# Kernel tuning notes

Measured on AMD Instinct MI355X. Metric: run time of the kernel, lower is better.

The kernel has to match this reference:

```python
import jax, jax.numpy as jnp
import numpy as np

B, N, D = 2, 2048, 256
H = 8
HD = D // H
SCALE = HD ** 0.5  # NOTE: source MULTIPLIES by sqrt(head_dim)
EPS = 1e-5
DFF = 4 * D


def setup_inputs() -> dict:
    key = jax.random.key(0)
    ks = jax.random.split(key, 9)
    s = lambda fan_in: 1.0 / np.sqrt(fan_in)
    return {
        "x": jax.random.normal(ks[0], (B, N, D), dtype=jnp.float32),
        # weights stored [in, out] (transposed torch Linear)
        "qkv_w": jax.random.normal(ks[1], (D, 3 * D), dtype=jnp.float32) * s(D),
        "proj_w": jax.random.normal(ks[2], (D, D), dtype=jnp.float32) * s(D),
        "proj_b": jax.random.normal(ks[3], (D,), dtype=jnp.float32) * 0.01,
        "fc1_w": jax.random.normal(ks[4], (D, DFF), dtype=jnp.float32) * s(D),
        "fc1_b": jax.random.normal(ks[5], (DFF,), dtype=jnp.float32) * 0.01,
        "fc2_w": jax.random.normal(ks[6], (DFF, D), dtype=jnp.float32) * s(DFF),
        "fc2_b": jax.random.normal(ks[7], (D,), dtype=jnp.float32) * 0.01,
        "ln1_g": jnp.ones((D,), dtype=jnp.float32),
        "ln1_b": jnp.zeros((D,), dtype=jnp.float32),
    }


def _layernorm(x, g, b):
    mu = jnp.mean(x, axis=-1, keepdims=True)
    var = jnp.mean(jnp.square(x - mu), axis=-1, keepdims=True)
    return (x - mu) * jax.lax.rsqrt(var + EPS) * g + b


def reference(x, qkv_w, proj_w, proj_b, fc1_w, fc1_b, fc2_w, fc2_b, ln1_g, ln1_b):
    b, n, d = x.shape
    # --- MHA ---
    qkv = (x @ qkv_w).reshape(b, n, 3, H, HD)
    q = qkv[:, :, 0].transpose(0, 2, 1, 3)  # [B,H,N,HD]
    k = qkv[:, :, 1].transpose(0, 2, 1, 3)
    v = qkv[:, :, 2].transpose(0, 2, 1, 3)
    att = jnp.einsum("bhqd,bhkd->bhqk", q, k) * SCALE  # multiplied, per source
    att = jax.nn.softmax(att, axis=-1)
    out = jnp.einsum("bhqk,bhkd->bhqd", att, v)
    out = out.transpose(0, 2, 1, 3).reshape(b, n, d)
    out = out @ proj_w + proj_b
    # --- post-norm residual ---
    net = _layernorm(out + x, ln1_g, ln1_b)
    shortcut = net
    # --- MLP (NO activation in source forward) ---
    net = (net @ fc1_w + fc1_b) @ fc2_w + fc2_b
    return net + shortcut
```

## Files before the change

kernel.cpp:

```cpp
#include <hip/hip_runtime.h>


typedef __attribute__((ext_vector_type(8))) short short8;
typedef __attribute__((ext_vector_type(4))) short short4v;
typedef __attribute__((ext_vector_type(8))) _Float16 half8;
typedef __attribute__((ext_vector_type(4))) _Float16 half4;
typedef __attribute__((ext_vector_type(2))) __fp16 fp16x2;
typedef __attribute__((ext_vector_type(4))) float floatx4;
typedef __attribute__((ext_vector_type(2))) unsigned int uint2v;
typedef unsigned short u16;

#define MFMAG(a,b,c)  __builtin_amdgcn_mfma_f32_16x16x32_f16((a),(b),(c),0,0,0)
#if __has_builtin(__builtin_amdgcn_mfma_f32_16x16x16_f16)
#define MFMAPV(a,b,c) __builtin_amdgcn_mfma_f32_16x16x16_f16((a),(b),(c),0,0,0)
#else
#define MFMAPV(a,b,c) __builtin_amdgcn_mfma_f32_16x16x16f16((a),(b),(c),0,0,0)
#endif
#define CLF 8.1615404f

#if __has_builtin(__builtin_amdgcn_exp2f)
#define EX2(x) __builtin_amdgcn_exp2f(x)
#else
#define EX2(x) exp2f(x)
#endif

__device__ __forceinline__ float bf2f(u16 u) { return __uint_as_float(((unsigned)u) << 16); }
__device__ __forceinline__ float h2f(u16 u) { _Float16 h = *(_Float16*)&u; return (float)h; }
__device__ __forceinline__ u16 f2h(float f) { _Float16 h = (_Float16)f; return *(u16*)&h; }
__device__ __forceinline__ unsigned pkh2(float a, float b) {
#if __has_builtin(__builtin_amdgcn_cvt_pkrtz)
  fp16x2 h = __builtin_amdgcn_cvt_pkrtz(a, b);
  return *(unsigned*)&h;
#else
  return (unsigned)f2h(a) | ((unsigned)f2h(b) << 16);
#endif
}
__device__ __forceinline__ void gll16(const void* g, void* l) {
  __builtin_amdgcn_global_load_lds((const __attribute__((address_space(1))) void*)g,
                                   (__attribute__((address_space(3))) void*)l, 16, 0, 0);
}

__global__ __launch_bounds__(256) void qkvprep_k(
    const void* __restrict__ x, const void* __restrict__ qkv_w,
    const void* __restrict__ proj_w, const void* __restrict__ fc1_w,
    const void* __restrict__ fc2_w, const void* __restrict__ proj_b,
    const void* __restrict__ fc1_b, const void* __restrict__ fc2_b,
    const void* __restrict__ ln_g, const void* __restrict__ ln_b,
    u16* __restrict__ wt_proj, u16* __restrict__ wt_fc1, u16* __restrict__ wt_fc2,
    u16* __restrict__ b_proj, u16* __restrict__ b_fc1, u16* __restrict__ b_fc2,
    u16* __restrict__ g_ln, u16* __restrict__ bb_ln,
    u16* __restrict__ vt, u16* __restrict__ qf, u16* __restrict__ kf)
{
  __shared__ __align__(16) u16 lds[9728];
  const int tid = threadIdx.x;
  const int lane = tid & 63;
  const float probe = bf2f(((const u16*)qkv_w)[lane]);
  const bool f32 = __ballot(!(fabsf(probe) < 1000.0f)) != 0ull;
  const int bid = blockIdx.x;
  #define RD(p, i) (f32 ? ((const float*)(p))[i] : bf2f(((const u16*)(p))[i]))

  if (bid >= 768) {
    int idx = bid - 768;
    if (idx < 144) {
      u16 (*tr)[70] = (u16(*)[70])lds;
      const void* src; u16* dst; int Ns, Kt, tk, tn;
      if (idx < 16)      { src = proj_w; dst = wt_proj; Ns = 256;  Kt = 256;
                           tk = idx & 3;  tn = idx >> 2; }
      else if (idx < 80) { idx -= 16; src = fc1_w; dst = wt_fc1; Ns = 1024; Kt = 256;
                           tk = idx & 3;  tn = idx >> 2; }
      else               { idx -= 80; src = fc2_w; dst = wt_fc2; Ns = 256;  Kt = 1024;
                           tk = idx & 15; tn = idx >> 4; }
      const int k0 = tk * 64, n0v = tn * 64;
      const int r = tid >> 6, c = tid & 63;
#pragma unroll
      for (int p = 0; p < 16; ++p) {
        const int k = k0 + p * 4 + r;
        tr[c][p * 4 + r] = f2h(RD(src, (size_t)k * Ns + n0v + c));
      }
      __syncthreads();
#pragma unroll
      for (int p = 0; p < 16; ++p) {
        const int n = n0v + p * 4 + r;
        dst[(size_t)n * Kt + k0 + c] = tr[p * 4 + r][c];
      }
    } else {
      const int j = (idx - 144) * 256 + tid;
      if (j < 256)       b_proj[j]        = f2h(RD(proj_b, j));
      else if (j < 1280) b_fc1[j - 256]   = f2h(RD(fc1_b, j - 256));
      else if (j < 1536) b_fc2[j - 1280]  = f2h(RD(fc2_b, j - 1280));
      else if (j < 1792) g_ln[j - 1536]   = f2h(RD(ln_g, j - 1536));
      else if (j < 2048) bb_ln[j - 1792]  = f2h(RD(ln_b, j - 1792));
    }
    return;
  }
  #undef RD

  u16 (*As)[40] = (u16(*)[40])lds;
  u16 (*Bs)[40] = (u16(*)[40])(lds + 2560);
  u16* Vt = lds + 5120;
  const int mb = bid / 12, nb = bid % 12;
  const int m0 = mb * 64, n0 = nb * 64;
  const int wid = tid >> 6;
  const int wm = (wid >> 1) * 32, wn = (wid & 1) * 32;
  const int lm = lane & 15, quad = lane >> 4;

  floatx4 zero = {0.f, 0.f, 0.f, 0.f};
  floatx4 acc[2][2] = {{zero, zero}, {zero, zero}};

  const int arow = tid >> 2, aoff = (tid & 3) * 8;
  const int bn = tid & 63, bk8 = (tid >> 6) * 8;

  short8 rah, rbh;
  auto ld = [&](int kk) {
    if (f32) {
      const float* xp = (const float*)x + (size_t)(m0 + arow) * 256 + kk + aoff;
      floatx4 a0 = *(const floatx4*)xp;
      floatx4 a1 = *(const floatx4*)(xp + 4);
#pragma unroll
      for (int j = 0; j < 4; ++j) {
        rah[j]     = (short)f2h(a0[j]);
        rah[4 + j] = (short)f2h(a1[j]);
      }
      const float* wp = (const float*)qkv_w + (size_t)(kk + bk8) * 768 + n0 + bn;
#pragma unroll
      for (int j = 0; j < 8; ++j) rbh[j] = (short)f2h(wp[(size_t)j * 768]);
    } else {
      short8 a = *(const short8*)((const u16*)x + (size_t)(m0 + arow) * 256 + kk + aoff);
#pragma unroll
      for (int j = 0; j < 8; ++j) rah[j] = (short)f2h(bf2f((u16)a[j]));
      const u16* wp = (const u16*)qkv_w + (size_t)(kk + bk8) * 768 + n0 + bn;
#pragma unroll
      for (int j = 0; j < 8; ++j) rbh[j] = (short)f2h(bf2f(wp[(size_t)j * 768]));
    }
  };
  ld(0);
  for (int k0 = 0; k0 < 256; k0 += 32) {
    if (k0) __syncthreads();
    *(short8*)&As[arow][aoff] = rah;
    *(short8*)&Bs[bn][bk8] = rbh;
    __syncthreads();
    if (k0 + 32 < 256) ld(k0 + 32);
    half8 fa[2], fb[2];
#pragma unroll
    for (int t = 0; t < 2; ++t) {
      fa[t] = *(const half8*)&As[wm + t * 16 + lm][quad * 8];
      fb[t] = *(const half8*)&Bs[wn + t * 16 + lm][quad * 8];
    }
#pragma unroll
    for (int i = 0; i < 2; ++i)
#pragma unroll
      for (int j = 0; j < 2; ++j)
        acc[i][j] = MFMAG(fa[i], fb[j], acc[i][j]);
  }

  if (n0 >= 512) {
    __syncthreads();
#pragma unroll
    for (int i = 0; i < 2; ++i)
#pragma unroll
      for (int j = 0; j < 2; ++j)
#pragma unroll
        for (int r = 0; r < 4; ++r)
          Vt[(wn + j * 16 + lm) * 72 + wm + i * 16 + quad * 4 + r] = f2h(acc[i][j][r]);
    __syncthreads();
    const int bb = m0 >> 11, n = m0 & 2047;
#pragma unroll
    for (int pass = 0; pass < 2; ++pass) {
      const int dl = (tid >> 3) + pass * 32;
      const int oct = tid & 7;
      const int col = n0 - 512 + dl;
      const int d = col & 31, hh = col >> 5;
      short8 v = *(const short8*)&Vt[dl * 72 + oct * 8];
      *(short8*)&vt[(size_t)((bb * 8 + hh) * 32 + d) * 2048 + n + oct * 8] = v;
    }
    return;
  }

#pragma unroll
  for (int i = 0; i < 2; ++i) {
    const int rowb = m0 + wm + i * 16 + quad * 4;
#pragma unroll
    for (int j = 0; j < 2; ++j) {
      const int col = n0 + wn + j * 16 + lm;
#pragma unroll
      for (int r = 0; r < 4; ++r) {
        const int row = rowb + r;
        const u16 hv = f2h(acc[i][j][r]);
        if (col < 256) qf[(size_t)row * 256 + col] = hv;
        else           kf[(size_t)row * 256 + (col - 256)] = hv;
      }
    }
  }
}

__global__ __launch_bounds__(256) void prep_k(
    const void* __restrict__ x, const void* __restrict__ qkv_w,
    const void* __restrict__ proj_w, const void* __restrict__ fc1_w,
    const void* __restrict__ fc2_w, const void* __restrict__ proj_b,
    const void* __restrict__ fc1_b, const void* __restrict__ fc2_b,
    const void* __restrict__ ln_g, const void* __restrict__ ln_b,
    u16* __restrict__ x_f, u16* __restrict__ wq_f,
    u16* __restrict__ wt_proj, u16* __restrict__ wt_fc1, u16* __restrict__ wt_fc2,
    u16* __restrict__ b_proj, u16* __restrict__ b_fc1, u16* __restrict__ b_fc2,
    u16* __restrict__ g_ln, u16* __restrict__ bb_ln)
{
  __shared__ u16 tr[64][70];
  const int lane = threadIdx.x & 63;
  const float probe = bf2f(((const u16*)qkv_w)[lane]);
  const bool f32 = __ballot(!(fabsf(probe) < 1000.0f)) != 0ull;
  const int bid = blockIdx.x, tid = threadIdx.x;
  #define RD(p, i) (f32 ? ((const float*)(p))[i] : bf2f(((const u16*)(p))[i]))
  if (bid < 1024) {
    const size_t i = (size_t)bid * 1024 + tid * 4;
    const u16 o0 = f2h(RD(x, i)),     o1 = f2h(RD(x, i + 1));
    const u16 o2 = f2h(RD(x, i + 2)), o3 = f2h(RD(x, i + 3));
    short4v sv = {(short)o0, (short)o1, (short)o2, (short)o3};
    *(short4v*)&x_f[i] = sv;
  } else if (bid < 1216) {
    int idx = bid - 1024;
    const void* src; u16* dst; int Ns, Kt, tk, tn;
    if (idx < 48)       { src = qkv_w;  dst = wq_f;    Ns = 768;  Kt = 256;
                          tk = idx & 3;  tn = idx >> 2; }
    else if (idx < 64)  { idx -= 48;  src = proj_w; dst = wt_proj; Ns = 256; Kt = 256;
                          tk = idx & 3;  tn = idx >> 2; }
    else if (idx < 128) { idx -= 64;  src = fc1_w;  dst = wt_fc1;  Ns = 1024; Kt = 256;
                          tk = idx & 3;  tn = idx >> 2; }
    else                { idx -= 128; src = fc2_w;  dst = wt_fc2;  Ns = 256;  Kt = 1024;
                          tk = idx & 15; tn = idx >> 4; }
    const int k0 = tk * 64, n0 = tn * 64;
    const int r = tid >> 6, c = tid & 63;
#pragma unroll
    for (int p = 0; p < 16; ++p) {
      const int k = k0 + p * 4 + r;
      tr[c][p * 4 + r] = f2h(RD(src, (size_t)k * Ns + n0 + c));
    }
    __syncthreads();
#pragma unroll
    for (int p = 0; p < 16; ++p) {
      const int n = n0 + p * 4 + r;
      dst[(size_t)n * Kt + k0 + c] = tr[p * 4 + r][c];
    }
  } else {
    const int j = (bid - 1216) * 256 + tid;
    if (j < 256)       b_proj[j]        = f2h(RD(proj_b, j));
    else if (j < 1280) b_fc1[j - 256]   = f2h(RD(fc1_b, j - 256));
    else if (j < 1536) b_fc2[j - 1280]  = f2h(RD(fc2_b, j - 1280));
    else if (j < 1792) g_ln[j - 1536]   = f2h(RD(ln_g, j - 1536));
    else if (j < 2048) bb_ln[j - 1792]  = f2h(RD(ln_b, j - 1792));
  }
  #undef RD
}

template<int TW, int EPI, bool BIAS, bool RES, bool COMB>
__global__ __launch_bounds__(256) void gemm_k(
    const u16* __restrict__ A, const u16* __restrict__ Bt, const u16* __restrict__ A2,
    const u16* __restrict__ bias, const u16* __restrict__ res,
    void* __restrict__ out0, u16* __restrict__ aux1, u16* __restrict__ aux3,
    const float* __restrict__ muc,
    int M, int Nn, int K)
{
  constexpr int BT = TW * 32;
  constexpr int NC = TW / 2;
  __shared__ __align__(16) u16 As[BT][40];
  __shared__ __align__(16) u16 Bs[BT][40];
  __shared__ __align__(16) u16 Vt[(EPI == 2) ? 64 * 72 : 1];
  const int tid = threadIdx.x;
  const int m0 = blockIdx.y * BT, n0 = blockIdx.x * BT;
  const int wid = tid >> 6, lane = tid & 63;
  const int wm = (wid >> 1) * (TW * 16), wn = (wid & 1) * (TW * 16);
  const int lm = lane & 15, quad = lane >> 4;

  floatx4 zero = {0.f, 0.f, 0.f, 0.f};
  floatx4 acc[TW][TW];
#pragma unroll
  for (int i = 0; i < TW; ++i)
#pragma unroll
    for (int j = 0; j < TW; ++j) acc[i][j] = zero;

  auto comb8 = [&](int t, int col8) -> short8 {
    const size_t o = (size_t)t * 256 + col8;
    const int h = col8 >> 5;
    const float m0_ = muc[t * 8 + h],          m1_ = muc[32768 + t * 8 + h];
    const float m2_ = muc[65536 + t * 8 + h],  m3_ = muc[98304 + t * 8 + h];
    const float M = fmaxf(fmaxf(m0_, m1_), fmaxf(m2_, m3_));
    float w0 = EX2(m0_ - M), w1 = EX2(m1_ - M), w2 = EX2(m2_ - M), w3 = EX2(m3_ - M);
    const float inv = 1.f / (w0 + w1 + w2 + w3);
    w0 *= inv; w1 *= inv; w2 *= inv; w3 *= inv;
    short8 a0 = *(const short8*)&A[o],  a1 = *(const short8*)&A[o + 1048576];
    short8 a2 = *(const short8*)&A2[o], a3 = *(const short8*)&A2[o + 1048576];
    float v[8];
#pragma unroll
    for (int j = 0; j < 8; ++j)
      v[j] = w0 * h2f((u16)a0[j]) + w1 * h2f((u16)a1[j])
           + w2 * h2f((u16)a2[j]) + w3 * h2f((u16)a3[j]);
    uint2v uu0 = {pkh2(v[0], v[1]), pkh2(v[2], v[3])};
    uint2v uu1 = {pkh2(v[4], v[5]), pkh2(v[6], v[7])};
    short8 r;
    *(uint2v*)&r = uu0; *((uint2v*)&r + 1) = uu1;
    return r;
  };

  int srow[NC], soff[NC];
#pragma unroll
  for (int c = 0; c < NC; ++c) {
    const int cid = tid * NC + c;
    srow[c] = cid >> 2; soff[c] = (cid & 3) * 8;
  }

  short8 ra0[NC], rb0[NC];
  auto ld = [&](int kk) {
#pragma unroll
    for (int c = 0; c < NC; ++c) {
      rb0[c] = *(const short8*)&Bt[(size_t)(n0 + srow[c]) * K + kk + soff[c]];
      if (COMB) ra0[c] = comb8(m0 + srow[c], kk + soff[c]);
      else      ra0[c] = *(const short8*)&A[(size_t)(m0 + srow[c]) * K + kk + soff[c]];
    }
  };
  ld(0);
  for (int k0 = 0; k0 < K; k0 += 32) {
    if (k0) __syncthreads();
#pragma unroll
    for (int c = 0; c < NC; ++c) {
      *(short8*)&As[srow[c]][soff[c]] = ra0[c];
      *(short8*)&Bs[srow[c]][soff[c]] = rb0[c];
    }
    __syncthreads();
    if (k0 + 32 < K) ld(k0 + 32);
    half8 fa[TW], fb[TW];
#pragma unroll
    for (int t = 0; t < TW; ++t) {
      fa[t] = *(const half8*)&As[wm + t * 16 + lm][quad * 8];
      fb[t] = *(const half8*)&Bs[wn + t * 16 + lm][quad * 8];
    }
#pragma unroll
    for (int i = 0; i < TW; ++i)
#pragma unroll
      for (int j = 0; j < TW; ++j)
        acc[i][j] = MFMAG(fa[i], fb[j], acc[i][j]);
  }

  if (EPI == 2 && n0 >= 512) {
    __syncthreads();
#pragma unroll
    for (int i = 0; i < TW; ++i)
#pragma unroll
      for (int j = 0; j < TW; ++j)
#pragma unroll
        for (int r = 0; r < 4; ++r)
          Vt[(wn + j * 16 + lm) * 72 + wm + i * 16 + quad * 4 + r] = f2h(acc[i][j][r]);
    __syncthreads();
    const int bb = m0 >> 11, n = m0 & 2047;
#pragma unroll
    for (int pass = 0; pass < 2; ++pass) {
      const int dl = (tid >> 3) + pass * 32;
      const int oct = tid & 7;
      const int col = n0 - 512 + dl;
      const int d = col & 31, hh = col >> 5;
      short8 v = *(const short8*)&Vt[dl * 72 + oct * 8];
      *(short8*)&((u16*)out0)[(size_t)((bb * 8 + hh) * 32 + d) * 2048 + n + oct * 8] = v;
    }
    return;
  }

#pragma unroll
  for (int i = 0; i < TW; ++i) {
    const int rowb = m0 + wm + i * 16 + quad * 4;
#pragma unroll
    for (int j = 0; j < TW; ++j) {
      const int col = n0 + wn + j * 16 + lm;
      const float bv = BIAS ? h2f(bias[col]) : 0.f;
#pragma unroll
      for (int r = 0; r < 4; ++r) {
        const int row = rowb + r;
        float v = acc[i][j][r] + bv;
        const size_t o = (size_t)row * Nn + col;
        if (RES) v += h2f(res[o]);
        if (EPI == 0) {
          ((float*)out0)[o] = v;
        } else if (EPI == 1) {
          ((u16*)out0)[o] = f2h(v);
        } else {
          if (col < 256) aux1[(size_t)row * 256 + col] = f2h(v);
          else           aux3[(size_t)row * 256 + (col - 256)] = f2h(v);
        }
      }
    }
  }
}

__global__ __launch_bounds__(512) void gemm8_k(
    const u16* __restrict__ A, const u16* __restrict__ Bt,
    const u16* __restrict__ bias, const u16* __restrict__ res,
    float* __restrict__ out0, int Nn, int K)
{
  __shared__ __align__(16) u16 As[64][40];
  __shared__ __align__(16) u16 Bs[64][40];
  const int tid = threadIdx.x;
  const int m0 = blockIdx.y * 64, n0 = blockIdx.x * 64;
  const int wid = tid >> 6, lane = tid & 63;
  const int wm = (wid & 3) * 16, wn = (wid >> 2) * 32;
  const int lm = lane & 15, quad = lane >> 4;

  floatx4 zero = {0.f, 0.f, 0.f, 0.f};
  floatx4 acc0 = zero, acc1 = zero;

  const int sgrp = tid >> 8, stid = tid & 255;
  const int srow = stid >> 2, soff = (stid & 3) * 8;
  const u16* sp = sgrp ? Bt : A;
  const int sbase = sgrp ? n0 : m0;

  short8 rr;
  rr = *(const short8*)&sp[(size_t)(sbase + srow) * K + soff];
  for (int k0 = 0; k0 < K; k0 += 32) {
    if (k0) __syncthreads();
    if (sgrp) *(short8*)&Bs[srow][soff] = rr;
    else      *(short8*)&As[srow][soff] = rr;
    __syncthreads();
    if (k0 + 32 < K)
      rr = *(const short8*)&sp[(size_t)(sbase + srow) * K + k0 + 32 + soff];
    half8 fa = *(const half8*)&As[wm + lm][quad * 8];
    half8 fb0 = *(const half8*)&Bs[wn + lm][quad * 8];
    half8 fb1 = *(const half8*)&Bs[wn + 16 + lm][quad * 8];
    acc0 = MFMAG(fa, fb0, acc0);
    acc1 = MFMAG(fa, fb1, acc1);
  }

  const int rowb = m0 + wm + quad * 4;
  const int col0 = n0 + wn + lm, col1 = col0 + 16;
  const float bv0 = h2f(bias[col0]), bv1 = h2f(bias[col1]);
#pragma unroll
  for (int r = 0; r < 4; ++r) {
    const int row = rowb + r;
    const size_t o0 = (size_t)row * Nn + col0;
    const size_t o1 = (size_t)row * Nn + col1;
    out0[o0] = acc0[r] + bv0 + h2f(res[o0]);
    out0[o1] = acc1[r] + bv1 + h2f(res[o1]);
  }
}

__global__ __launch_bounds__(512) void projln8_k(
    const u16* __restrict__ A,
    const u16* __restrict__ A2,
    const u16* __restrict__ Bt,
    const u16* __restrict__ bias,
    const void* __restrict__ xraw,
    const void* __restrict__ probew,
    const u16* __restrict__ g, const u16* __restrict__ bb,
    const float* __restrict__ muc,
    u16* __restrict__ net)
{
  __shared__ __align__(16) u16 As[16][40];
  __shared__ __align__(16) u16 Bs[256][40];
  __shared__ float ss[8][16], ssq[8][16];
  const int tid = threadIdx.x;
  const int m0 = blockIdx.x * 16;
  const int wid = tid >> 6, lane = tid & 63;
  const int lm = lane & 15, quad = lane >> 4;
  const float probe = bf2f(((const u16*)probew)[lane]);
  const bool f32 = __ballot(!(fabsf(probe) < 1000.0f)) != 0ull;

  floatx4 zero = {0.f, 0.f, 0.f, 0.f};
  floatx4 acc0 = zero, acc1 = zero;

  auto comb8 = [&](int t, int col8) -> short8 {
    const size_t o = (size_t)t * 256 + col8;
    const int h = col8 >> 5;
    const float m0_ = muc[t * 8 + h],          m1_ = muc[32768 + t * 8 + h];
    const float m2_ = muc[65536 + t * 8 + h],  m3_ = muc[98304 + t * 8 + h];
    const float M = fmaxf(fmaxf(m0_, m1_), fmaxf(m2_, m3_));
    float w0 = EX2(m0_ - M), w1 = EX2(m1_ - M), w2 = EX2(m2_ - M), w3 = EX2(m3_ - M);
    const float inv = 1.f / (w0 + w1 + w2 + w3);
    w0 *= inv; w1 *= inv; w2 *= inv; w3 *= inv;
    short8 a0 = *(const short8*)&A[o],  a1 = *(const short8*)&A[o + 1048576];
    short8 a2 = *(const short8*)&A2[o], a3 = *(const short8*)&A2[o + 1048576];
    float v[8];
#pragma unroll
    for (int j = 0; j < 8; ++j)
      v[j] = w0 * h2f((u16)a0[j]) + w1 * h2f((u16)a1[j])
           + w2 * h2f((u16)a2[j]) + w3 * h2f((u16)a3[j]);
    uint2v uu0 = {pkh2(v[0], v[1]), pkh2(v[2], v[3])};
    uint2v uu1 = {pkh2(v[4], v[5]), pkh2(v[6], v[7])};
    short8 r;
    *(uint2v*)&r = uu0; *((uint2v*)&r + 1) = uu1;
    return r;
  };

  const int arow = lane >> 2, aoff = (lane & 3) * 8;
  int brow0 = wid * 32 + (lane >> 2), brow1 = brow0 + 16;
  const int boff = (lane & 3) * 8;

  short8 ra, rb0, rb1;
  if (wid == 0) ra = comb8(m0 + arow, aoff);
  rb0 = *(const short8*)&Bt[(size_t)brow0 * 256 + boff];
  rb1 = *(const short8*)&Bt[(size_t)brow1 * 256 + boff];

  for (int k0 = 0; k0 < 256; k0 += 32) {
    if (k0) __syncthreads();
    if (wid == 0) *(short8*)&As[arow][aoff] = ra;
    *(short8*)&Bs[brow0][boff] = rb0;
    *(short8*)&Bs[brow1][boff] = rb1;
    __syncthreads();
    if (k0 + 32 < 256) {
      if (wid == 0) ra = comb8(m0 + arow, k0 + 32 + aoff);
      rb0 = *(const short8*)&Bt[(size_t)brow0 * 256 + k0 + 32 + boff];
      rb1 = *(const short8*)&Bt[(size_t)brow1 * 256 + k0 + 32 + boff];
    }
    half8 fa = *(const half8*)&As[lm][quad * 8];
    half8 fb0 = *(const half8*)&Bs[wid * 32 + lm][quad * 8];
    half8 fb1 = *(const half8*)&Bs[wid * 32 + 16 + lm][quad * 8];
    acc0 = MFMAG(fa, fb0, acc0);
    acc1 = MFMAG(fa, fb1, acc1);
  }

  const int col0 = wid * 32 + lm, col1 = col0 + 16;
  const float bv0 = h2f(bias[col0]), bv1 = h2f(bias[col1]);
  float s[4], sq[4], v0[4], v1[4];
#pragma unroll
  for (int r = 0; r < 4; ++r) {
    const int row = quad * 4 + r;
    const size_t o0 = (size_t)(m0 + row) * 256 + col0;
    const size_t o1 = (size_t)(m0 + row) * 256 + col1;
    const float x0 = f32 ? ((const float*)xraw)[o0] : bf2f(((const u16*)xraw)[o0]);
    const float x1 = f32 ? ((const float*)xraw)[o1] : bf2f(((const u16*)xraw)[o1]);
    const float a = acc0[r] + bv0 + h2f(f2h(x0));
    const float b = acc1[r] + bv1 + h2f(f2h(x1));
    v0[r] = a; v1[r] = b;
    s[r] = a + b; sq[r] = a * a + b * b;
  }
#pragma unroll
  for (int d = 1; d < 16; d <<= 1)
#pragma unroll
    for (int r = 0; r < 4; ++r) {
      s[r] += __shfl_xor(s[r], d);
      sq[r] += __shfl_xor(sq[r], d);
    }
  if (lm == 0)
#pragma unroll
    for (int r = 0; r < 4; ++r) { ss[wid][quad * 4 + r] = s[r]; ssq[wid][quad * 4 + r] = sq[r]; }
  __syncthreads();
#pragma unroll
  for (int r = 0; r < 4; ++r) {
    const int row = quad * 4 + r;
    float ts = 0.f, tq = 0.f;
#pragma unroll
    for (int w = 0; w < 8; ++w) { ts += ss[w][row]; tq += ssq[w][row]; }
    const float mean = ts * (1.f / 256.f);
    const float var = tq * (1.f / 256.f) - mean * mean;
    const float is = rsqrtf(var + 1e-5f);
    net[(size_t)(m0 + row) * 256 + col0] =
        f2h((v0[r] - mean) * is * h2f(g[col0]) + h2f(bb[col0]));
    net[(size_t)(m0 + row) * 256 + col1] =
        f2h((v1[r] - mean) * is * h2f(g[col1]) + h2f(bb[col1]));
  }
}

template<int CHUNKS>
__global__ __launch_bounds__(256) void attn_k(
    const u16* __restrict__ qf16, const u16* __restrict__ kf16,
    const u16* __restrict__ vt, u16* __restrict__ outp, u16* __restrict__ out23,
    float* __restrict__ mu)
{
  __shared__ __align__(16) u16 Ks[2][64][32];
  __shared__ __align__(16) u16 Vs[2][32][64];
  const int tid = threadIdx.x, wid = tid >> 6, lane = tid & 63;
  const int lm = lane & 15, quad = lane >> 4;
  const int bid = blockIdx.x;
  const int chunk = (CHUNKS > 1) ? (bid >> 9) : 0;
  const int qblk = bid & 31, bh = (bid >> 5) & 15;
  const int b = bh >> 3, h = bh & 7;
  const int q0 = qblk * 64 + wid * 16;
  const size_t tb = (size_t)b * 2048;
  const int NT = 32 / CHUNKS;
  const int kofs = chunk * (2048 / CHUNKS);

  half8 qh;
  { size_t off = (tb + q0 + lm) * 256 + h * 32 + quad * 8;
    qh = *(const half8*)&qf16[off]; }

  const int kkey = tid >> 2, kg = tid & 3;
  const size_t kb = (tb + kofs + kkey) * 256 + h * 32 + kg * 8;
  const int vd = tid >> 3, vp = tid & 7, vk8 = vp ^ (vd & 7);
  const size_t vb = (size_t)(bh * 32 + vd) * 2048 + kofs + vk8 * 8;

  gll16(kf16 + kb, (u16*)Ks + tid * 8);
  gll16(vt  + vb,  (u16*)Vs + tid * 8);

  float mrun = -1e30f, lrun = 0.f;
  floatx4 o0 = {0.f,0.f,0.f,0.f}, o1 = {0.f,0.f,0.f,0.f};

  for (int kt = 0; kt < NT; ++kt) {
    const int buf = kt & 1;
    __syncthreads();
    if (kt < NT - 1) {
      const int nb = (buf ^ 1) * 2048;
      const size_t ko = (size_t)(kt + 1) * 16384;
      const size_t vo = (size_t)(kt + 1) * 64;
      gll16(kf16 + kb + ko, (u16*)Ks + nb + tid * 8);
      gll16(vt  + vb + vo,  (u16*)Vs + nb + tid * 8);
    }

    floatx4 z[4];
#pragma unroll
    for (int kf = 0; kf < 4; ++kf) {
      half8 khf = *(const half8*)&Ks[buf][kf * 16 + lm][quad * 8];
      floatx4 zz = {0.f,0.f,0.f,0.f};
      z[kf] = MFMAG(khf, qh, zz);
    }
    float zm = fmaxf(fmaxf(fmaxf(z[0][0], z[0][1]), fmaxf(z[0][2], z[0][3])),
               fmaxf(fmaxf(z[1][0], z[1][1]), fmaxf(z[1][2], z[1][3])));
    zm = fmaxf(zm, fmaxf(fmaxf(fmaxf(z[2][0], z[2][1]), fmaxf(z[2][2], z[2][3])),
                   fmaxf(fmaxf(z[3][0], z[3][1]), fmaxf(z[3][2], z[3][3]))));
    zm = fmaxf(zm, __shfl_xor(zm, 16));
    zm = fmaxf(zm, __shfl_xor(zm, 32));
    const float mn = fmaxf(mrun, zm);
    const float alpha = EX2((mrun - mn) * CLF);
    const float mc = mn * CLF;
    mrun = mn;
    float ls = 0.f;
    half4 pb[4];
#pragma unroll
    for (int kf = 0; kf < 4; ++kf) {
      const float p0 = EX2(__builtin_fmaf(z[kf][0], CLF, -mc));
      const float p1 = EX2(__builtin_fmaf(z[kf][1], CLF, -mc));
      const float p2 = EX2(__builtin_fmaf(z[kf][2], CLF, -mc));
      const float p3 = EX2(__builtin_fmaf(z[kf][3], CLF, -mc));
      ls += (p0 + p1) + (p2 + p3);
      uint2v uu = {pkh2(p0, p1), pkh2(p2, p3)};
      pb[kf] = *(half4*)&uu;
    }
    ls += __shfl_xor(ls, 16);
    ls += __shfl_xor(ls, 32);
    lrun = lrun * alpha + ls;
#pragma unroll
    for (int r = 0; r < 4; ++r) { o0[r] *= alpha; o1[r] *= alpha; }
    const u16* vbase = (const u16*)Vs + buf * 2048;
#pragma unroll
    for (int kf = 0; kf < 4; ++kf) {
      const int k8 = 2 * kf + (quad >> 1);
      const int d0 = lm, d1 = 16 + lm;
      half4 vf0 = *(const half4*)(vbase + (d0 * 8 + (k8 ^ (d0 & 7))) * 8 + (quad & 1) * 4);
      half4 vf1 = *(const half4*)(vbase + (d1 * 8 + (k8 ^ (d1 & 7))) * 8 + (quad & 1) * 4);
      o0 = MFMAPV(vf0, pb[kf], o0);
      o1 = MFMAPV(vf1, pb[kf], o1);
    }
  }
  const float inv = 1.0f / lrun;
  const size_t tok = tb + q0 + lm;
  u16* dst = ((CHUNKS > 2 && chunk >= 2) ? out23 : outp) + (size_t)(chunk & 1) * 1048576;
  const size_t rowo = tok * 256 + h * 32;
#pragma unroll
  for (int r = 0; r < 4; ++r) {
    dst[rowo + quad * 4 + r]      = f2h(o0[r] * inv);
    dst[rowo + 16 + quad * 4 + r] = f2h(o1[r] * inv);
  }
  if (CHUNKS > 1 && quad == 0)
    mu[chunk * 32768 + tok * 8 + h] = __builtin_fmaf(mrun, CLF, __log2f(lrun));
}

template<int CHUNKS>
__global__ __launch_bounds__(256) void combine_k(u16* __restrict__ d,
                                                 const u16* __restrict__ e,
                                                 const float* __restrict__ mu)
{
  const int t = blockIdx.x, c = threadIdx.x, h = c >> 5;
  const size_t o = (size_t)t * 256 + c;
  float m[CHUNKS];
  float M = -1e30f;
#pragma unroll
  for (int i = 0; i < CHUNKS; ++i) { m[i] = mu[i * 32768 + t * 8 + h]; M = fmaxf(M, m[i]); }
  float wsum = 0.f, acc = 0.f;
#pragma unroll
  for (int i = 0; i < CHUNKS; ++i) {
    const float w = EX2(m[i] - M);
    const u16 v = (i < 2) ? d[o + (size_t)i * 1048576] : e[o + (size_t)(i - 2) * 1048576];
    wsum += w; acc += w * h2f(v);
  }
  d[o] = f2h(acc / wsum);
}

__global__ __launch_bounds__(256) void ln_k(const float* __restrict__ pf,
                                            const u16* __restrict__ xh,
                                            const u16* __restrict__ g,
                                            const u16* __restrict__ bta,
                                            u16* __restrict__ net)
{
  const int t = blockIdx.x, c = threadIdx.x;
  const size_t o = (size_t)t * 256 + c;
  float v = pf[o] + h2f(xh[o]);
  float s = v, s2 = v * v;
#pragma unroll
  for (int d = 1; d < 64; d <<= 1) { s += __shfl_xor(s, d); s2 += __shfl_xor(s2, d); }
  __shared__ float ss[4], ss2[4];
  const int w = c >> 6;
  if ((c & 63) == 0) { ss[w] = s; ss2[w] = s2; }
  __syncthreads();
  s = ss[0] + ss[1] + ss[2] + ss[3];
  s2 = ss2[0] + ss2[1] + ss2[2] + ss2[3];
  const float mu = s * (1.f / 256.f);
  const float var = s2 * (1.f / 256.f) - mu * mu;
  const float is = rsqrtf(var + 1e-5f);
  net[o] = f2h((v - mu) * is * h2f(g[c]) + h2f(bta[c]));
}

extern "C" void kernel_launch(void* const* d_in, const int* in_sizes, int n_in,
                              void* d_out, int out_size, void* d_ws, size_t ws_size,
                              hipStream_t stream) {
  const void* x      = d_in[0];
  const void* qkv_w  = d_in[1];
  const void* proj_w = d_in[2];
  const void* proj_b = d_in[3];
  const void* fc1_w  = d_in[4];
  const void* fc1_b  = d_in[5];
  const void* fc2_w  = d_in[6];
  const void* fc2_b  = d_in[7];
  const void* ln_g   = d_in[8];
  const void* ln_b   = d_in[9];

  char* ws = (char*)d_ws;
  u16* b_proj  = (u16*)(ws + 4096);
  u16* b_fc1   = (u16*)(ws + 8192);
  u16* b_fc2   = (u16*)(ws + 12288);
  u16* g_ln    = (u16*)(ws + 16384);
  u16* bb_ln   = (u16*)(ws + 20480);
  u16* wq_f    = (u16*)(ws + 131072);
  u16* wt_proj = (u16*)(ws + 524288);
  u16* wt_fc1  = (u16*)(ws + 655360);
  u16* wt_fc2  = (u16*)(ws + 1179648);
  u16* x_f     = (u16*)(ws + 2097152);
  u16* q_f16   = (u16*)(ws + 4194304);
  u16* k_f16   = (u16*)(ws + 6291456);
  u16* vt      = (u16*)(ws + 8388608);
  float* mu    = (float*)(ws + 10485760);
  u16* out23   = (u16*)(ws + 11010048);
  u16* attn    = (u16*)d_out;

  u16* net4    = (u16*)(ws + 2097152);
  u16* hbuf4   = (u16*)(ws + 4194304);

  float* projf = (float*)(ws + 4194304);
  u16* net     = (u16*)(ws + 11010048);
  u16* hbuf    = (u16*)(ws + 2097152);

  const bool sk4 = ws_size >= 15204352;
  const bool sk2 = ws_size >= 11010048;

  if (sk4) {
    qkvprep_k<<<920, 256, 0, stream>>>(x, qkv_w, proj_w, fc1_w, fc2_w,
                                       proj_b, fc1_b, fc2_b, ln_g, ln_b,
                                       wt_proj, wt_fc1, wt_fc2,
                                       b_proj, b_fc1, b_fc2, g_ln, bb_ln,
                                       vt, q_f16, k_f16);
    attn_k<4><<<2048, 256, 0, stream>>>(q_f16, k_f16, vt, attn, out23, mu);
    projln8_k<<<256, 512, 0, stream>>>(attn, out23, wt_proj, b_proj, x, qkv_w,
                                       g_ln, bb_ln, mu, net4);
    gemm_k<2, 1, true, false, false><<<dim3(16, 64), 256, 0, stream>>>(
        net4, wt_fc1, nullptr, b_fc1, nullptr, hbuf4, nullptr, nullptr, nullptr,
        4096, 1024, 256);
    gemm8_k<<<dim3(4, 64), 512, 0, stream>>>(
        hbuf4, wt_fc2, b_fc2, net4, (float*)d_out, 256, 1024);
    return;
  }

  prep_k<<<1224, 256, 0, stream>>>(x, qkv_w, proj_w, fc1_w, fc2_w,
                                   proj_b, fc1_b, fc2_b, ln_g, ln_b,
                                   x_f, wq_f, wt_proj, wt_fc1, wt_fc2,
                                   b_proj, b_fc1, b_fc2, g_ln, bb_ln);
  gemm_k<2, 2, false, false, false><<<dim3(12, 64), 256, 0, stream>>>(
      x_f, wq_f, nullptr, nullptr, nullptr, vt, q_f16, k_f16, nullptr, 4096, 768, 256);
  if (sk2) {
    attn_k<2><<<1024, 256, 0, stream>>>(q_f16, k_f16, vt, attn, nullptr, mu);
    combine_k<2><<<4096, 256, 0, stream>>>(attn, nullptr, mu);
    gemm_k<2, 0, true, false, false><<<dim3(4, 64), 256, 0, stream>>>(
        attn, wt_proj, nullptr, b_proj, nullptr, projf, nullptr, nullptr, nullptr,
        4096, 256, 256);
  } else {
    attn_k<1><<<512, 256, 0, stream>>>(q_f16, k_f16, vt, attn, nullptr, nullptr);
    gemm_k<2, 0, true, false, false><<<dim3(4, 64), 256, 0, stream>>>(
        attn, wt_proj, nullptr, b_proj, nullptr, projf, nullptr, nullptr, nullptr,
        4096, 256, 256);
  }
  ln_k<<<4096, 256, 0, stream>>>(projf, x_f, g_ln, bb_ln, net);
  gemm_k<2, 1, true, false, false><<<dim3(16, 64), 256, 0, stream>>>(
      net, wt_fc1, nullptr, b_fc1, nullptr, hbuf, nullptr, nullptr, nullptr,
      4096, 1024, 256);
  gemm_k<2, 0, true, true, false><<<dim3(4, 64), 256, 0, stream>>>(
      hbuf, wt_fc2, nullptr, b_fc2, net, d_out, nullptr, nullptr, nullptr,
      4096, 256, 1024);
}
```

Baseline: 141.2 us.

## Fold linear MLP into single precomputed weight matrix and bias

The MLP has no activation, so fc1 and fc2 collapse into one 256x256 matrix (fc1_w·fc2_w) and a combined bias (fc1_b·fc2_w + fc2_b). Both are computed inside the prep kernel using extra MFMA blocks. The two large MLP GEMMs over 4096 rows become one 256-wide GEMM with residual. The fused weight is recomputed on every call and rounded to fp16, which changes the rounding behaviour.

```diff
diff --git a/kernel.cpp b/kernel.cpp
--- a/kernel.cpp
+++ b/kernel.cpp
@@ -46,9 +46,8 @@
     const void* __restrict__ fc2_w, const void* __restrict__ proj_b,
     const void* __restrict__ fc1_b, const void* __restrict__ fc2_b,
     const void* __restrict__ ln_g, const void* __restrict__ ln_b,
-    u16* __restrict__ wt_proj, u16* __restrict__ wt_fc1, u16* __restrict__ wt_fc2,
-    u16* __restrict__ b_proj, u16* __restrict__ b_fc1, u16* __restrict__ b_fc2,
-    u16* __restrict__ g_ln, u16* __restrict__ bb_ln,
+    u16* __restrict__ wt_proj, u16* __restrict__ wmlp, u16* __restrict__ bmlp,
+    u16* __restrict__ b_proj, u16* __restrict__ g_ln, u16* __restrict__ bb_ln,
     u16* __restrict__ vt, u16* __restrict__ qf, u16* __restrict__ kf)
 {
   __shared__ __align__(16) u16 lds[9728];
@@ -61,39 +60,91 @@
 
   if (bid >= 768) {
     int idx = bid - 768;
-    if (idx < 144) {
+    if (idx < 16) {
       u16 (*tr)[70] = (u16(*)[70])lds;
-      const void* src; u16* dst; int Ns, Kt, tk, tn;
-      if (idx < 16)      { src = proj_w; dst = wt_proj; Ns = 256;  Kt = 256;
-                           tk = idx & 3;  tn = idx >> 2; }
-      else if (idx < 80) { idx -= 16; src = fc1_w; dst = wt_fc1; Ns = 1024; Kt = 256;
-                           tk = idx & 3;  tn = idx >> 2; }
-      else               { idx -= 80; src = fc2_w; dst = wt_fc2; Ns = 256;  Kt = 1024;
-                           tk = idx & 15; tn = idx >> 4; }
+      const int tk = idx & 3, tn = idx >> 2;
       const int k0 = tk * 64, n0v = tn * 64;
       const int r = tid >> 6, c = tid & 63;
 #pragma unroll
       for (int p = 0; p < 16; ++p) {
         const int k = k0 + p * 4 + r;
-        tr[c][p * 4 + r] = f2h(RD(src, (size_t)k * Ns + n0v + c));
+        tr[c][p * 4 + r] = f2h(RD(proj_w, (size_t)k * 256 + n0v + c));
       }
       __syncthreads();
 #pragma unroll
       for (int p = 0; p < 16; ++p) {
         const int n = n0v + p * 4 + r;
-        dst[(size_t)n * Kt + k0 + c] = tr[p * 4 + r][c];
+        wt_proj[(size_t)n * 256 + k0 + c] = tr[p * 4 + r][c];
       }
+    } else if (idx < 32) {
+      idx -= 16;
+      const int tn = idx >> 2, tk2 = idx & 3;
+      const int n0v = tn * 64, k0v = tk2 * 64;
+      u16 (*As)[40] = (u16(*)[40])lds;
+      u16 (*Bs)[40] = (u16(*)[40])(lds + 2560);
+      const int wid = tid >> 6;
+      const int wm = (wid >> 1) * 32, wn = (wid & 1) * 32;
+      const int lm = lane & 15, quad = lane >> 4;
+      floatx4 zero = {0.f, 0.f, 0.f, 0.f};
+      floatx4 acc[2][2] = {{zero, zero}, {zero, zero}};
+      const int an = tid & 63, aj8 = (tid >> 6) * 8;
+      const int bk = tid >> 2, bj8 = (tid & 3) * 8;
+      short8 ra, rb;
+      auto ld = [&](int j0) {
+#pragma unroll
+        for (int jj = 0; jj < 8; ++jj)
+          ra[jj] = (short)f2h(RD(fc2_w, (size_t)(j0 + aj8 + jj) * 256 + n0v + an));
+#pragma unroll
+        for (int jj = 0; jj < 8; ++jj)
+          rb[jj] = (short)f2h(RD(fc1_w, (size_t)(k0v + bk) * 1024 + j0 + bj8 + jj));
+      };
+      ld(0);
+      for (int j0 = 0; j0 < 1024; j0 += 32) {
+        if (j0) __syncthreads();
+        *(short8*)&As[an][aj8] = ra;
+        *(short8*)&Bs[bk][bj8] = rb;
+        __syncthreads();
+        if (j0 + 32 < 1024) ld(j0 + 32);
+        half8 fa[2], fb[2];
+#pragma unroll
+        for (int t = 0; t < 2; ++t) {
+          fa[t] = *(const half8*)&As[wm + t * 16 + lm][quad * 8];
+          fb[t] = *(const half8*)&Bs[wn + t * 16 + lm][quad * 8];
+        }
+#pragma unroll
+        for (int i = 0; i < 2; ++i)
+#pragma unroll
+          for (int j = 0; j < 2; ++j)
+            acc[i][j] = MFMAG(fa[i], fb[j], acc[i][j]);
+      }
+#pragma unroll
+      for (int i = 0; i < 2; ++i) {
+        const int rown = n0v + wm + i * 16 + quad * 4;
+#pragma unroll
+        for (int j = 0; j < 2; ++j) {
+          const int colk = k0v + wn + j * 16 + lm;
+#pragma unroll
+          for (int r = 0; r < 4; ++r)
+            wmlp[(size_t)(rown + r) * 256 + colk] = f2h(acc[i][j][r]);
+        }
+      }
+    } else if (idx < 36) {
+      const int q = idx - 32;
+      const int n = q * 64 + (tid >> 2), jg = tid & 3;
+      float s = 0.f;
+#pragma unroll 8
+      for (int j = jg; j < 1024; j += 4)
+        s += RD(fc1_b, j) * RD(fc2_w, (size_t)j * 256 + n);
+      s += __shfl_xor(s, 1);
+      s += __shfl_xor(s, 2);
+      if (jg == 0) bmlp[n] = f2h(s + RD(fc2_b, n));
     } else {
-      const int j = (idx - 144) * 256 + tid;
-      if (j < 256)       b_proj[j]        = f2h(RD(proj_b, j));
-      else if (j < 1280) b_fc1[j - 256]   = f2h(RD(fc1_b, j - 256));
-      else if (j < 1536) b_fc2[j - 1280]  = f2h(RD(fc2_b, j - 1280));
-      else if (j < 1792) g_ln[j - 1536]   = f2h(RD(ln_g, j - 1536));
-      else if (j < 2048) bb_ln[j - 1792]  = f2h(RD(ln_b, j - 1792));
+      b_proj[tid] = f2h(RD(proj_b, tid));
+      g_ln[tid]   = f2h(RD(ln_g, tid));
+      bb_ln[tid]  = f2h(RD(ln_b, tid));
     }
     return;
   }
-  #undef RD
 
   u16 (*As)[40] = (u16(*)[40])lds;
   u16 (*Bs)[40] = (u16(*)[40])(lds + 2560);
@@ -152,6 +203,7 @@
       for (int j = 0; j < 2; ++j)
         acc[i][j] = MFMAG(fa[i], fb[j], acc[i][j]);
   }
+  #undef RD
 
   if (n0 >= 512) {
     __syncthreads();
@@ -388,56 +440,6 @@
   }
 }
 
-__global__ __launch_bounds__(512) void gemm8_k(
-    const u16* __restrict__ A, const u16* __restrict__ Bt,
-    const u16* __restrict__ bias, const u16* __restrict__ res,
-    float* __restrict__ out0, int Nn, int K)
-{
-  __shared__ __align__(16) u16 As[64][40];
-  __shared__ __align__(16) u16 Bs[64][40];
-  const int tid = threadIdx.x;
-  const int m0 = blockIdx.y * 64, n0 = blockIdx.x * 64;
-  const int wid = tid >> 6, lane = tid & 63;
-  const int wm = (wid & 3) * 16, wn = (wid >> 2) * 32;
-  const int lm = lane & 15, quad = lane >> 4;
-
-  floatx4 zero = {0.f, 0.f, 0.f, 0.f};
-  floatx4 acc0 = zero, acc1 = zero;
-
-  const int sgrp = tid >> 8, stid = tid & 255;
-  const int srow = stid >> 2, soff = (stid & 3) * 8;
-  const u16* sp = sgrp ? Bt : A;
-  const int sbase = sgrp ? n0 : m0;
-
-  short8 rr;
-  rr = *(const short8*)&sp[(size_t)(sbase + srow) * K + soff];
-  for (int k0 = 0; k0 < K; k0 += 32) {
-    if (k0) __syncthreads();
-    if (sgrp) *(short8*)&Bs[srow][soff] = rr;
-    else      *(short8*)&As[srow][soff] = rr;
-    __syncthreads();
-    if (k0 + 32 < K)
-      rr = *(const short8*)&sp[(size_t)(sbase + srow) * K + k0 + 32 + soff];
-    half8 fa = *(const half8*)&As[wm + lm][quad * 8];
-    half8 fb0 = *(const half8*)&Bs[wn + lm][quad * 8];
-    half8 fb1 = *(const half8*)&Bs[wn + 16 + lm][quad * 8];
-    acc0 = MFMAG(fa, fb0, acc0);
-    acc1 = MFMAG(fa, fb1, acc1);
-  }
-
-  const int rowb = m0 + wm + quad * 4;
-  const int col0 = n0 + wn + lm, col1 = col0 + 16;
-  const float bv0 = h2f(bias[col0]), bv1 = h2f(bias[col1]);
-#pragma unroll
-  for (int r = 0; r < 4; ++r) {
-    const int row = rowb + r;
-    const size_t o0 = (size_t)row * Nn + col0;
-    const size_t o1 = (size_t)row * Nn + col1;
-    out0[o0] = acc0[r] + bv0 + h2f(res[o0]);
-    out0[o1] = acc1[r] + bv1 + h2f(res[o1]);
-  }
-}
-
 __global__ __launch_bounds__(512) void projln8_k(
     const u16* __restrict__ A,
     const u16* __restrict__ A2,
@@ -719,6 +721,7 @@
   char* ws = (char*)d_ws;
   u16* b_proj  = (u16*)(ws + 4096);
   u16* b_fc1   = (u16*)(ws + 8192);
+  u16* bmlp    = (u16*)(ws + 12288);
   u16* b_fc2   = (u16*)(ws + 12288);
   u16* g_ln    = (u16*)(ws + 16384);
   u16* bb_ln   = (u16*)(ws + 20480);
@@ -726,6 +729,7 @@
   u16* wt_proj = (u16*)(ws + 524288);
   u16* wt_fc1  = (u16*)(ws + 655360);
   u16* wt_fc2  = (u16*)(ws + 1179648);
+  u16* wmlp    = (u16*)(ws + 1703936);
   u16* x_f     = (u16*)(ws + 2097152);
   u16* q_f16   = (u16*)(ws + 4194304);
   u16* k_f16   = (u16*)(ws + 6291456);
@@ -735,7 +739,6 @@
   u16* attn    = (u16*)d_out;
 
   u16* net4    = (u16*)(ws + 2097152);
-  u16* hbuf4   = (u16*)(ws + 4194304);
 
   float* projf = (float*)(ws + 4194304);
   u16* net     = (u16*)(ws + 11010048);
@@ -745,19 +748,17 @@
   const bool sk2 = ws_size >= 11010048;
 
   if (sk4) {
-    qkvprep_k<<<920, 256, 0, stream>>>(x, qkv_w, proj_w, fc1_w, fc2_w,
+    qkvprep_k<<<805, 256, 0, stream>>>(x, qkv_w, proj_w, fc1_w, fc2_w,
                                        proj_b, fc1_b, fc2_b, ln_g, ln_b,
-                                       wt_proj, wt_fc1, wt_fc2,
-                                       b_proj, b_fc1, b_fc2, g_ln, bb_ln,
+                                       wt_proj, wmlp, bmlp,
+                                       b_proj, g_ln, bb_ln,
                                        vt, q_f16, k_f16);
     attn_k<4><<<2048, 256, 0, stream>>>(q_f16, k_f16, vt, attn, out23, mu);
     projln8_k<<<256, 512, 0, stream>>>(attn, out23, wt_proj, b_proj, x, qkv_w,
                                        g_ln, bb_ln, mu, net4);
-    gemm_k<2, 1, true, false, false><<<dim3(16, 64), 256, 0, stream>>>(
-        net4, wt_fc1, nullptr, b_fc1, nullptr, hbuf4, nullptr, nullptr, nullptr,
-        4096, 1024, 256);
-    gemm8_k<<<dim3(4, 64), 512, 0, stream>>>(
-        hbuf4, wt_fc2, b_fc2, net4, (float*)d_out, 256, 1024);
+    gemm_k<2, 0, true, true, false><<<dim3(4, 64), 256, 0, stream>>>(
+        net4, wmlp, nullptr, bmlp, net4, d_out, nullptr, nullptr, nullptr,
+        4096, 256, 256);
     return;
   }
 
```

After: 169.6 us. +20.2%, slower.
